# Kernel tuning notes

Measured on AMD Instinct MI355X. Metric: run time of the kernel, lower is better.

## Reference

```python
import jax, jax.numpy as jnp
import numpy as np

N = 50000      # nodes
E = 800000     # edges
NUM_STATIC = 8
T = 24         # dynamic seq len (in_features - num_static)
LH = 64        # lstm_hidden
C = 32         # n_hidden (per-head out channels)
H = 4          # heads
NC = 4         # num_classes
IN_GAT = LH + NUM_STATIC  # 72


def _uniform(key, shape, scale):
    return jax.random.uniform(key, shape, jnp.float32, -scale, scale)


def setup_inputs() -> dict:
    key = jax.random.key(0)
    ks = jax.random.split(key, 32)
    s1 = 1.0 / np.sqrt(LH)
    inp = {
        'x': jax.random.normal(ks[0], (N, NUM_STATIC + T), jnp.float32),
        'edge_index': jax.random.randint(ks[1], (2, E), 0, N, jnp.int64),
        'edge_attr': jax.random.uniform(ks[2], (E, 1), jnp.float32),
        # LSTM layer 0 (input_size=1), layer 1 (input_size=LH); gate order i,f,g,o
        'w_ih0': _uniform(ks[3], (4 * LH, 1), s1),
        'w_hh0': _uniform(ks[4], (4 * LH, LH), s1),
        'b_ih0': _uniform(ks[5], (4 * LH,), s1),
        'b_hh0': _uniform(ks[6], (4 * LH,), s1),
        'w_ih1': _uniform(ks[7], (4 * LH, LH), s1),
        'w_hh1': _uniform(ks[8], (4 * LH, LH), s1),
        'b_ih1': _uniform(ks[9], (4 * LH,), s1),
        'b_hh1': _uniform(ks[10], (4 * LH,), s1),
        # GATConv params (PyG: glorot lin, att vectors; bias zeros-init but randomize)
        'lin_w': _uniform(ks[11], (H * C, IN_GAT), np.sqrt(6.0 / (IN_GAT + H * C))),
        'lin_edge_w': _uniform(ks[12], (H * C, 1), np.sqrt(6.0 / (1 + H * C))),
        'att_src': _uniform(ks[13], (H, C), np.sqrt(6.0 / (C + 1))),
        'att_dst': _uniform(ks[14], (H, C), np.sqrt(6.0 / (C + 1))),
        'att_edge': _uniform(ks[15], (H, C), np.sqrt(6.0 / (C + 1))),
        'gat_bias': _uniform(ks[16], (H * C,), 0.1),
        # final Linear
        'fc_w': _uniform(ks[17], (NC, H * C), 1.0 / np.sqrt(H * C)),
        'fc_b': _uniform(ks[18], (NC,), 1.0 / np.sqrt(H * C)),
    }
    return inp


def _lstm_layer(x_seq, w_ih, w_hh, b_ih, b_hh):
    # x_seq: [N, T, D] -> hs: [N, T, LH]
    xw = jnp.einsum('ntd,gd->ntg', x_seq, w_ih) + b_ih + b_hh  # [N,T,4LH]
    n = x_seq.shape[0]
    h0 = jnp.zeros((n, w_hh.shape[1]), x_seq.dtype)

    def step(carry, xt):
        h, c = carry
        g = xt + h @ w_hh.T
        i, f, gg, o = jnp.split(g, 4, axis=-1)
        c = jax.nn.sigmoid(f) * c + jax.nn.sigmoid(i) * jnp.tanh(gg)
        h = jax.nn.sigmoid(o) * jnp.tanh(c)
        return (h, c), h

    _, hs = jax.lax.scan(step, (h0, h0), jnp.swapaxes(xw, 0, 1))
    return jnp.swapaxes(hs, 0, 1)


def reference(x, edge_index, edge_attr,
              w_ih0, w_hh0, b_ih0, b_hh0, w_ih1, w_hh1, b_ih1, b_hh1,
              lin_w, lin_edge_w, att_src, att_dst, att_edge, gat_bias,
              fc_w, fc_b):
    static = x[:, :NUM_STATIC]
    dyn = x[:, NUM_STATIC:, None]                      # [N,T,1]
    h1 = _lstm_layer(dyn, w_ih0, w_hh0, b_ih0, b_hh0)  # [N,T,LH] (eval: no dropout)
    h2 = _lstm_layer(h1, w_ih1, w_hh1, b_ih1, b_hh1)
    combined = jnp.concatenate([h2[:, -1, :], static], axis=1)  # [N, LH+NUM_STATIC]

    # --- GATConv (PyG defaults: add_self_loops=True, fill_value='mean') ---
    n = combined.shape[0]
    loop = jnp.arange(n, dtype=edge_index.dtype)
    src = jnp.concatenate([edge_index[0], loop])
    dst = jnp.concatenate([edge_index[1], loop])
    ea_mean = jnp.mean(edge_attr, axis=0, keepdims=True)        # [1,1]
    ea = jnp.concatenate([edge_attr, jnp.broadcast_to(ea_mean, (n, 1))], axis=0)

    xl = (combined @ lin_w.T).reshape(n, H, C)                  # [N,H,C]
    a_src = jnp.einsum('nhc,hc->nh', xl, att_src)               # [N,H]
    a_dst = jnp.einsum('nhc,hc->nh', xl, att_dst)
    e_emb = (ea @ lin_edge_w.T).reshape(-1, H, C)               # [Et,H,C]
    a_edge = jnp.einsum('ehc,hc->eh', e_emb, att_edge)          # [Et,H]

    logits = jax.nn.leaky_relu(a_src[src] + a_dst[dst] + a_edge, 0.2)  # [Et,H]
    m = jax.ops.segment_max(logits, dst, num_segments=n)
    ex = jnp.exp(logits - m[dst])
    denom = jax.ops.segment_sum(ex, dst, num_segments=n)
    alpha = ex / (denom[dst] + 1e-16)                           # [Et,H] (eval: no dropout)

    msg = xl[src] * alpha[:, :, None]                           # [Et,H,C]
    out = jax.ops.segment_sum(msg, dst, num_segments=n)         # [N,H,C]
    out = out.reshape(n, H * C) + gat_bias

    out = jax.nn.elu(out)
    return jax.nn.relu(out @ fc_w.T + fc_b)                     # [N,NC]
```

## Files before the change

kernel.cpp:

```cpp
#include <hip/hip_runtime.h>
#include <cstdint>

#define TT 24

typedef _Float16 half8 __attribute__((ext_vector_type(8)));
typedef float f32x4 __attribute__((ext_vector_type(4)));

static __device__ __forceinline__ float fsig(float x){
  float e = __builtin_amdgcn_exp2f(-1.44269504f*x);
  return __builtin_amdgcn_rcpf(1.0f + e);
}
static __device__ __forceinline__ float ftanh(float x){
  float e = __builtin_amdgcn_exp2f(-2.88539008f*x);
  return fmaf(2.0f, __builtin_amdgcn_rcpf(1.0f + e), -1.0f);
}
static __device__ __forceinline__ float lrelu(float x){ return x > 0.f ? x : 0.2f*x; }

static __device__ __forceinline__ int swzh(int b){ return b ^ (((b>>7)&7)<<4); }

__global__ void kPrep(const float* __restrict__ w_hh0, const float* __restrict__ w_ih1,
                      const float* __restrict__ w_hh1, const float* __restrict__ lin_w,
                      const float* __restrict__ lin_edge_w, const float* __restrict__ att_edge,
                      unsigned short* __restrict__ Bf,
                      float* __restrict__ linwT, float* __restrict__ cE)
{
  int gid = blockIdx.x*256 + threadIdx.x;
  if (gid < 49152){
    int mat = gid / 16384;
    int r = gid - mat*16384;
    int c = r>>13, nt = (r>>9)&15, l = (r>>3)&63, j = r&7;
    int k = c*32 + (l>>4)*8 + j;
    int col = nt*16 + (l&15);
    const float* wsrc = (mat==0) ? w_hh0 : (mat==1 ? w_ih1 : w_hh1);
    float v = wsrc[col*64 + k];
    union { _Float16 f; unsigned short u; } cv;
    cv.f = (_Float16)v;
    Bf[gid] = cv.u;
  }
  int g2 = gid - 49152;
  if (g2 >= 0 && g2 < 72*128){
    int k = g2 >> 7, ch = g2 & 127;
    linwT[g2] = lin_w[ch*72 + k];
  }
  if (gid >= 58368 && gid < 58372){
    int h = gid - 58368;
    float s = 0.f;
    for (int c=0;c<32;c++) s += lin_edge_w[h*32+c]*att_edge[h*32+c];
    cE[h] = s;
  }
}

__global__ __launch_bounds__(512) void kAB(const float* __restrict__ x,
    const unsigned short* __restrict__ Bf,
    const float* __restrict__ w_ih0, const float* __restrict__ b_ih0, const float* __restrict__ b_hh0,
    const float* __restrict__ b_ih1, const float* __restrict__ b_hh1,
    float* __restrict__ h2last, int N)
{
  __shared__ __align__(16) unsigned short sB[49152];
  __shared__ __align__(16) unsigned short sH1[4096];
  __shared__ __align__(16) unsigned short sH2[4096];
  __shared__ float sX[64*25];
  const int tid = threadIdx.x;
  const int wid = tid>>6, l = tid&63;
  const int wq = wid&3, wm = wid>>2;
  const int lr = l&15, lg = l>>4;
  const int nb = blockIdx.x*64;

  for (int i=tid; i<6144; i+=512)
    ((uint4*)sB)[i] = ((const uint4*)Bf)[i];
  for (int i=tid;i<1536;i+=512){
    int m = i/24, tt = i - m*24;
    int n = nb + m;
    sX[m*25+tt] = (n<N) ? x[(size_t)n*32 + 8 + tt] : 0.f;
  }
  for (int i=tid;i<4096;i+=512){ sH1[i]=0; sH2[i]=0; }

  float wih[4], bb0[4], bb1[4];
  #pragma unroll
  for (int nt=0;nt<4;nt++){
    int col = nt*64 + wq*16 + lr;
    wih[nt] = w_ih0[col];
    bb0[nt] = b_ih0[col] + b_hh0[col];
    bb1[nt] = b_ih1[col] + b_hh1[col];
  }
  float cc0[8], cc1[8];
  #pragma unroll
  for (int i=0;i<8;i++){ cc0[i]=0.f; cc1[i]=0.f; }
  __syncthreads();

  const char* h1B = (const char*)sH1;
  const char* h2B = (const char*)sH2;

  for (int t=0;t<TT;t++){
    f32x4 acc[2][4];
    #pragma unroll
    for (int mt=0;mt<2;mt++){
      #pragma unroll
      for (int r=0;r<4;r++){
        float xv = sX[(wm*32 + mt*16 + lg*4 + r)*25 + t];
        #pragma unroll
        for (int nt=0;nt<4;nt++) acc[mt][nt][r] = fmaf(xv, wih[nt], bb0[nt]);
      }
    }
    #pragma unroll
    for (int c=0;c<2;c++){
      half8 a[2];
      #pragma unroll
      for (int mt=0;mt<2;mt++){
        int by = swzh((wm*32 + mt*16 + lr)*128 + c*64 + lg*16);
        a[mt] = *(const half8*)(h1B + by);
      }
      #pragma unroll
      for (int nt=0;nt<4;nt++){
        half8 b = *(const half8*)&sB[((c*16 + nt*4 + wq)<<9) + l*8];
        #pragma unroll
        for (int mt=0;mt<2;mt++)
          acc[mt][nt] = __builtin_amdgcn_mfma_f32_16x16x32_f16(a[mt], b, acc[mt][nt], 0,0,0);
      }
    }
    __syncthreads();
    #pragma unroll
    for (int mt=0;mt<2;mt++){
      #pragma unroll
      for (int r=0;r<4;r++){
        int idx = mt*4+r, nd = wm*32 + mt*16 + lg*4 + r;
        float ig = fsig(acc[mt][0][r]), fg = fsig(acc[mt][1][r]);
        float gg = ftanh(acc[mt][2][r]), og = fsig(acc[mt][3][r]);
        cc0[idx] = fg*cc0[idx] + ig*gg;
        float h = og*ftanh(cc0[idx]);
        union { _Float16 f; unsigned short u; } cv; cv.f = (_Float16)h;
        *(unsigned short*)((char*)sH1 + swzh(nd*128 + (wq*16+lr)*2)) = cv.u;
      }
    }
    __syncthreads();
    #pragma unroll
    for (int mt=0;mt<2;mt++)
      #pragma unroll
      for (int nt=0;nt<4;nt++)
        #pragma unroll
        for (int r=0;r<4;r++) acc[mt][nt][r] = bb1[nt];
    #pragma unroll
    for (int c4=0;c4<4;c4++){
      const char* srcA = (c4<2) ? h1B : h2B;
      int cc = c4&1;
      int matB = (c4<2) ? 32 : 64;
      half8 a[2];
      #pragma unroll
      for (int mt=0;mt<2;mt++){
        int by = swzh((wm*32 + mt*16 + lr)*128 + cc*64 + lg*16);
        a[mt] = *(const half8*)(srcA + by);
      }
      #pragma unroll
      for (int nt=0;nt<4;nt++){
        half8 b = *(const half8*)&sB[((matB + cc*16 + nt*4 + wq)<<9) + l*8];
        #pragma unroll
        for (int mt=0;mt<2;mt++)
          acc[mt][nt] = __builtin_amdgcn_mfma_f32_16x16x32_f16(a[mt], b, acc[mt][nt], 0,0,0);
      }
    }
    __syncthreads();
    #pragma unroll
    for (int mt=0;mt<2;mt++){
      #pragma unroll
      for (int r=0;r<4;r++){
        int idx = mt*4+r, nd = wm*32 + mt*16 + lg*4 + r;
        float ig = fsig(acc[mt][0][r]), fg = fsig(acc[mt][1][r]);
        float gg = ftanh(acc[mt][2][r]), og = fsig(acc[mt][3][r]);
        cc1[idx] = fg*cc1[idx] + ig*gg;
        float h = og*ftanh(cc1[idx]);
        union { _Float16 f; unsigned short u; } cv; cv.f = (_Float16)h;
        *(unsigned short*)((char*)sH2 + swzh(nd*128 + (wq*16+lr)*2)) = cv.u;
        if (t == TT-1){
          int n = nb + nd;
          if (n < N) h2last[(size_t)n*64 + wq*16 + lr] = h;
        }
      }
    }
  }
}

__global__ __launch_bounds__(256) void kXL(const float* __restrict__ h2last, const float* __restrict__ x,
    const float* __restrict__ linwT, const float* __restrict__ att_src, const float* __restrict__ att_dst,
    float* __restrict__ xl, float* __restrict__ a_src, float* __restrict__ a_dst, int N)
{
  __shared__ float sLW[72*128];
  __shared__ float sC[16*72];
  const int tid = threadIdx.x;
  const int nb0 = blockIdx.x * 16;
  for (int i = tid*4; i < 9216; i += 1024)
    *(float4*)&sLW[i] = *(const float4*)&linwT[i];
  for (int i = tid; i < 16*64; i += 256){
    int m = i >> 6, k = i & 63; int n = nb0 + m;
    sC[m*72 + k] = (n < N) ? h2last[(size_t)n*64 + k] : 0.f;
  }
  if (tid < 128){
    int m = tid >> 3, j = tid & 7; int n = nb0 + m;
    sC[m*72 + 64 + j] = (n < N) ? x[(size_t)n*32 + j] : 0.f;
  }
  __syncthreads();
  const int ch = tid & 127, half = tid >> 7;
  float acc[8];
  #pragma unroll
  for (int m=0;m<8;m++) acc[m]=0.f;
  for (int k=0;k<72;k++){
    float w = sLW[k*128 + ch];
    #pragma unroll
    for (int m=0;m<8;m++) acc[m] += w * sC[(half*8+m)*72 + k];
  }
  float aS = att_src[ch], aD = att_dst[ch];
  int h = ch >> 5;
  #pragma unroll
  for (int m=0;m<8;m++){
    int n = nb0 + half*8 + m;
    float v = acc[m];
    float ps = v*aS, pd = v*aD;
    #pragma unroll
    for (int d=1; d<32; d<<=1){ ps += __shfl_xor(ps, d); pd += __shfl_xor(pd, d); }
    if (n < N){
      xl[(size_t)n*128 + ch] = v;
      if ((ch & 31) == 0){ a_src[n*4 + h] = ps; a_dst[n*4 + h] = pd; }
    }
  }
}

__global__ void kEa(const float* __restrict__ ea, float* __restrict__ acc, int E){
  int gid = blockIdx.x*blockDim.x + threadIdx.x;
  float s = 0.f;
  for (int i = gid; i < E; i += gridDim.x*blockDim.x) s += ea[i];
  #pragma unroll
  for (int d=1; d<64; d<<=1) s += __shfl_xor(s, d);
  if ((threadIdx.x & 63) == 0) atomicAdd(acc, s);
}

__global__ void kDeg(const int* __restrict__ dst, int* __restrict__ deg, int E, int N){
  int e = blockIdx.x*256 + threadIdx.x;
  if (e < E){
    unsigned d = (unsigned)dst[e];
    if (d < (unsigned)N) atomicAdd(&deg[d], 1);
  }
}

__global__ __launch_bounds__(1024) void kScan(const int* __restrict__ deg, int* __restrict__ ptrA,
                                              int* __restrict__ cursor, int N){
  __shared__ int sWS[16];
  __shared__ int sWO[16];
  const int tid = threadIdx.x;
  const int C = (N + 1 + 1023) / 1024;
  const int i0 = tid * C;
  int local = 0;
  for (int i = i0; i < i0 + C && i < N; i++) local += deg[i];
  int lane = tid & 63, wv = tid >> 6;
  int v = local;
  #pragma unroll
  for (int d=1; d<64; d<<=1){ int u = __shfl_up(v, d); if (lane >= d) v += u; }
  if (lane == 63) sWS[wv] = v;
  __syncthreads();
  if (tid < 16){
    int s = sWS[tid];
    int vv = s;
    #pragma unroll
    for (int d=1; d<16; d<<=1){ int u = __shfl_up(vv, d); if (tid >= d) vv += u; }
    sWO[tid] = vv - s;
  }
  __syncthreads();
  int run = sWO[wv] + (v - local);
  for (int i = i0; i < i0 + C; i++){
    if (i <= N){
      ptrA[i] = run;
      if (i < N){ cursor[i] = run; run += deg[i]; }
    }
  }
}

__global__ void kFill(const int* __restrict__ dst, int* __restrict__ cursor,
                      int* __restrict__ csr, int E, int N){
  int e = blockIdx.x*256 + threadIdx.x;
  if (e < E){
    unsigned d = (unsigned)dst[e];
    if (d < (unsigned)N){ int p = atomicAdd(&cursor[d], 1); csr[p] = e; }
  }
}

__global__ __launch_bounds__(256) void kAgg(const float* __restrict__ xl, const float* __restrict__ a_src,
    const float* __restrict__ a_dst, const int* __restrict__ esrc, const float* __restrict__ eattr,
    const int* __restrict__ ptrA, const int* __restrict__ csr, const float* __restrict__ cE,
    const float* __restrict__ eacc, const float* __restrict__ gat_bias, const float* __restrict__ fc_w,
    const float* __restrict__ fc_b, float* __restrict__ out, int N, int E)
{
  const int n = blockIdx.x*4 + (threadIdx.x >> 6);
  const int lane = threadIdx.x & 63;
  if (n >= N) return;
  float4 cEv = *(const float4*)cE;
  float eam = eacc[0] / (float)E;
  float4 ad  = *(const float4*)&a_dst[n*4];
  float4 asn = *(const float4*)&a_src[n*4];
  float sl0 = lrelu(asn.x + ad.x + eam*cEv.x);
  float sl1 = lrelu(asn.y + ad.y + eam*cEv.y);
  float sl2 = lrelu(asn.z + ad.z + eam*cEv.z);
  float sl3 = lrelu(asn.w + ad.w + eam*cEv.w);
  float mx0=sl0, mx1=sl1, mx2=sl2, mx3=sl3;
  const int p0 = ptrA[n], p1 = ptrA[n+1];
  for (int i = p0 + lane; i < p1; i += 64){
    int e = csr[i];
    int s = esrc[e];
    float ev = eattr[e];
    float4 av = *(const float4*)&a_src[s*4];
    mx0 = fmaxf(mx0, lrelu(av.x + ad.x + ev*cEv.x));
    mx1 = fmaxf(mx1, lrelu(av.y + ad.y + ev*cEv.y));
    mx2 = fmaxf(mx2, lrelu(av.z + ad.z + ev*cEv.z));
    mx3 = fmaxf(mx3, lrelu(av.w + ad.w + ev*cEv.w));
  }
  #pragma unroll
  for (int d=1; d<64; d<<=1){
    mx0 = fmaxf(mx0, __shfl_xor(mx0,d));
    mx1 = fmaxf(mx1, __shfl_xor(mx1,d));
    mx2 = fmaxf(mx2, __shfl_xor(mx2,d));
    mx3 = fmaxf(mx3, __shfl_xor(mx3,d));
  }
  const int ch0 = lane, ch1 = lane + 64;
  const int h0 = lane >> 5;
  float adh0 = h0 ? ad.y : ad.x,  adh1 = h0 ? ad.w : ad.z;
  float ceh0 = h0 ? cEv.y : cEv.x, ceh1 = h0 ? cEv.w : cEv.z;
  float mxh0 = h0 ? mx1 : mx0,    mxh1 = h0 ? mx3 : mx2;
  float slh0 = h0 ? sl1 : sl0,    slh1 = h0 ? sl3 : sl2;
  float pse0 = __expf(slh0 - mxh0), pse1 = __expf(slh1 - mxh1);
  float den0 = pse0, den1 = pse1;
  float acc0 = pse0 * xl[(size_t)n*128 + ch0];
  float acc1 = pse1 * xl[(size_t)n*128 + ch1];
  for (int i = p0; i < p1; i++){
    int e = csr[i];
    int s = esrc[e];
    float ev = eattr[e];
    float4 av = *(const float4*)&a_src[s*4];
    float avh0 = h0 ? av.y : av.x;
    float avh1 = h0 ? av.w : av.z;
    float pp0 = __expf(lrelu(avh0 + adh0 + ev*ceh0) - mxh0);
    float pp1 = __expf(lrelu(avh1 + adh1 + ev*ceh1) - mxh1);
    den0 += pp0; den1 += pp1;
    acc0 += pp0 * xl[(size_t)s*128 + ch0];
    acc1 += pp1 * xl[(size_t)s*128 + ch1];
  }
  float v0 = acc0/(den0 + 1e-16f) + gat_bias[ch0];
  float v1 = acc1/(den1 + 1e-16f) + gat_bias[ch1];
  v0 = v0 > 0.f ? v0 : __expf(v0) - 1.f;
  v1 = v1 > 0.f ? v1 : __expf(v1) - 1.f;
  #pragma unroll
  for (int o=0;o<4;o++){
    float p = fc_w[o*128 + ch0]*v0 + fc_w[o*128 + ch1]*v1;
    #pragma unroll
    for (int d=1; d<64; d<<=1) p += __shfl_xor(p, d);
    if (lane == 0) out[(size_t)n*4 + o] = fmaxf(p + fc_b[o], 0.f);
  }
}

extern "C" void kernel_launch(void* const* d_in, const int* in_sizes, int n_in,
                              void* d_out, int out_size, void* d_ws, size_t ws_size,
                              hipStream_t stream)
{
  (void)n_in; (void)out_size; (void)ws_size;
  const float* x          = (const float*)d_in[0];
  const int*   eidx       = (const int*)d_in[1];
  const float* eattr      = (const float*)d_in[2];
  const float* w_ih0      = (const float*)d_in[3];
  const float* w_hh0      = (const float*)d_in[4];
  const float* b_ih0      = (const float*)d_in[5];
  const float* b_hh0      = (const float*)d_in[6];
  const float* w_ih1      = (const float*)d_in[7];
  const float* w_hh1      = (const float*)d_in[8];
  const float* b_ih1      = (const float*)d_in[9];
  const float* b_hh1      = (const float*)d_in[10];
  const float* lin_w      = (const float*)d_in[11];
  const float* lin_edge_w = (const float*)d_in[12];
  const float* att_src    = (const float*)d_in[13];
  const float* att_dst    = (const float*)d_in[14];
  const float* att_edge   = (const float*)d_in[15];
  const float* gat_bias   = (const float*)d_in[16];
  const float* fc_w       = (const float*)d_in[17];
  const float* fc_b       = (const float*)d_in[18];
  float* out = (float*)d_out;

  const int N = in_sizes[0] / 32;
  const int E = in_sizes[1] / 2;
  const int* esrc = eidx;
  const int* edst = eidx + E;

  float* ws = (float*)d_ws;
  size_t o = 0;
  unsigned short* Bfrag = (unsigned short*)(ws + o); o += 24576;
  float* linwT  = ws + o; o += 72*128;
  float* cE     = ws + o; o += 4;
  float* eacc   = ws + o; o += 4;
  float* h2last = ws + o; o += (size_t)N*64;
  float* xl     = ws + o; o += (size_t)N*128;
  float* a_src  = ws + o; o += (size_t)N*4;
  float* a_dst  = ws + o; o += (size_t)N*4;
  int* deg      = (int*)(ws + o); o += (size_t)N;
  int* ptrA     = (int*)(ws + o); o += (size_t)N + 1;
  int* cursor   = (int*)(ws + o); o += (size_t)N;
  int* csr      = (int*)(ws + o); o += (size_t)E;

  hipMemsetAsync(deg, 0, (size_t)N*4, stream);
  hipMemsetAsync(eacc, 0, 4, stream);
  kPrep<<<229, 256, 0, stream>>>(w_hh0, w_ih1, w_hh1, lin_w, lin_edge_w, att_edge,
                                 Bfrag, linwT, cE);
  kEa<<<512, 256, 0, stream>>>(eattr, eacc, E);
  kDeg<<<(E+255)/256, 256, 0, stream>>>(edst, deg, E, N);
  kScan<<<1, 1024, 0, stream>>>(deg, ptrA, cursor, N);
  kFill<<<(E+255)/256, 256, 0, stream>>>(edst, cursor, csr, E, N);

  kAB<<<(N+63)/64, 512, 0, stream>>>(x, Bfrag, w_ih0, b_ih0, b_hh0,
                                     b_ih1, b_hh1, h2last, N);

  kXL<<<(N+15)/16, 256, 0, stream>>>(h2last, x, linwT, att_src, att_dst, xl, a_src, a_dst, N);
  kAgg<<<(N+3)/4, 256, 0, stream>>>(xl, a_src, a_dst, esrc, eattr, ptrA, csr, cE, eacc,
                                    gat_bias, fc_w, fc_b, out, N, E);
}
```

Baseline: 844.6 us.

## Keep LSTM weights in registers and store GAT features as fp16

The LSTM kernel now holds all three fp16 weight fragment sets in registers instead of copying 96KB into shared memory per block. Blocks shrink to 32 nodes and 256 threads, so LDS use drops and more blocks can be resident. Separately, the node feature matrix xl is written as packed fp16 with the two head-halves interleaved, which halves the gather bandwidth in the aggregation kernel. The costs are higher register pressure (24 half8 weight fragments per thread) and reduced precision in the aggregated features.

```diff
diff --git a/kernel.cpp b/kernel.cpp
--- a/kernel.cpp
+++ b/kernel.cpp
@@ -17,6 +17,12 @@
 static __device__ __forceinline__ float lrelu(float x){ return x > 0.f ? x : 0.2f*x; }
 
 static __device__ __forceinline__ int swzh(int b){ return b ^ (((b>>7)&7)<<4); }
+static __device__ __forceinline__ float h2f_lo(unsigned u){
+  union { unsigned short s; _Float16 f; } c; c.s = (unsigned short)(u & 0xFFFF); return (float)c.f;
+}
+static __device__ __forceinline__ float h2f_hi(unsigned u){
+  union { unsigned short s; _Float16 f; } c; c.s = (unsigned short)(u >> 16); return (float)c.f;
+}
 
 __global__ void kPrep(const float* __restrict__ w_hh0, const float* __restrict__ w_ih1,
                       const float* __restrict__ w_hh1, const float* __restrict__ lin_w,
@@ -50,30 +56,37 @@
   }
 }
 
-__global__ __launch_bounds__(512) void kAB(const float* __restrict__ x,
+__global__ __launch_bounds__(256) void kAB(const float* __restrict__ x,
     const unsigned short* __restrict__ Bf,
     const float* __restrict__ w_ih0, const float* __restrict__ b_ih0, const float* __restrict__ b_hh0,
     const float* __restrict__ b_ih1, const float* __restrict__ b_hh1,
     float* __restrict__ h2last, int N)
 {
-  __shared__ __align__(16) unsigned short sB[49152];
-  __shared__ __align__(16) unsigned short sH1[4096];
-  __shared__ __align__(16) unsigned short sH2[4096];
-  __shared__ float sX[64*25];
+  __shared__ __align__(16) unsigned short sH1[2048];
+  __shared__ __align__(16) unsigned short sH2[2048];
+  __shared__ float sX[32*25];
   const int tid = threadIdx.x;
-  const int wid = tid>>6, l = tid&63;
-  const int wq = wid&3, wm = wid>>2;
+  const int wq = tid>>6, l = tid&63;
   const int lr = l&15, lg = l>>4;
-  const int nb = blockIdx.x*64;
-
-  for (int i=tid; i<6144; i+=512)
-    ((uint4*)sB)[i] = ((const uint4*)Bf)[i];
-  for (int i=tid;i<1536;i+=512){
+  const int nb = blockIdx.x*32;
+
+  for (int i=tid;i<768;i+=256){
     int m = i/24, tt = i - m*24;
     int n = nb + m;
     sX[m*25+tt] = (n<N) ? x[(size_t)n*32 + 8 + tt] : 0.f;
   }
-  for (int i=tid;i<4096;i+=512){ sH1[i]=0; sH2[i]=0; }
+  for (int i=tid;i<2048;i+=256){ sH1[i]=0; sH2[i]=0; }
+
+  half8 w0[2][4], w1i[2][4], w1h[2][4];
+  #pragma unroll
+  for (int c=0;c<2;c++){
+    #pragma unroll
+    for (int nt=0;nt<4;nt++){
+      w0 [c][nt] = *(const half8*)&Bf[(( 0 + c*16 + nt*4 + wq)<<9) + l*8];
+      w1i[c][nt] = *(const half8*)&Bf[((32 + c*16 + nt*4 + wq)<<9) + l*8];
+      w1h[c][nt] = *(const half8*)&Bf[((64 + c*16 + nt*4 + wq)<<9) + l*8];
+    }
+  }
 
   float wih[4], bb0[4], bb1[4];
   #pragma unroll
@@ -97,7 +110,7 @@
     for (int mt=0;mt<2;mt++){
       #pragma unroll
       for (int r=0;r<4;r++){
-        float xv = sX[(wm*32 + mt*16 + lg*4 + r)*25 + t];
+        float xv = sX[(mt*16 + lg*4 + r)*25 + t];
         #pragma unroll
         for (int nt=0;nt<4;nt++) acc[mt][nt][r] = fmaf(xv, wih[nt], bb0[nt]);
       }
@@ -106,16 +119,13 @@
     for (int c=0;c<2;c++){
       half8 a[2];
       #pragma unroll
-      for (int mt=0;mt<2;mt++){
-        int by = swzh((wm*32 + mt*16 + lr)*128 + c*64 + lg*16);
-        a[mt] = *(const half8*)(h1B + by);
-      }
+      for (int mt=0;mt<2;mt++)
+        a[mt] = *(const half8*)(h1B + swzh((mt*16+lr)*128 + c*64 + lg*16));
       #pragma unroll
       for (int nt=0;nt<4;nt++){
-        half8 b = *(const half8*)&sB[((c*16 + nt*4 + wq)<<9) + l*8];
         #pragma unroll
         for (int mt=0;mt<2;mt++)
-          acc[mt][nt] = __builtin_amdgcn_mfma_f32_16x16x32_f16(a[mt], b, acc[mt][nt], 0,0,0);
+          acc[mt][nt] = __builtin_amdgcn_mfma_f32_16x16x32_f16(a[mt], w0[c][nt], acc[mt][nt], 0,0,0);
       }
     }
     __syncthreads();
@@ -123,7 +133,7 @@
     for (int mt=0;mt<2;mt++){
       #pragma unroll
       for (int r=0;r<4;r++){
-        int idx = mt*4+r, nd = wm*32 + mt*16 + lg*4 + r;
+        int idx = mt*4+r, nd = mt*16 + lg*4 + r;
         float ig = fsig(acc[mt][0][r]), fg = fsig(acc[mt][1][r]);
         float gg = ftanh(acc[mt][2][r]), og = fsig(acc[mt][3][r]);
         cc0[idx] = fg*cc0[idx] + ig*gg;
@@ -142,17 +152,14 @@
     #pragma unroll
     for (int c4=0;c4<4;c4++){
       const char* srcA = (c4<2) ? h1B : h2B;
-      int cc = c4&1;
-      int matB = (c4<2) ? 32 : 64;
+      const int cc = c4&1;
       half8 a[2];
       #pragma unroll
-      for (int mt=0;mt<2;mt++){
-        int by = swzh((wm*32 + mt*16 + lr)*128 + cc*64 + lg*16);
-        a[mt] = *(const half8*)(srcA + by);
-      }
+      for (int mt=0;mt<2;mt++)
+        a[mt] = *(const half8*)(srcA + swzh((mt*16+lr)*128 + cc*64 + lg*16));
       #pragma unroll
       for (int nt=0;nt<4;nt++){
-        half8 b = *(const half8*)&sB[((matB + cc*16 + nt*4 + wq)<<9) + l*8];
+        half8 b = (c4<2) ? w1i[cc][nt] : w1h[cc][nt];
         #pragma unroll
         for (int mt=0;mt<2;mt++)
           acc[mt][nt] = __builtin_amdgcn_mfma_f32_16x16x32_f16(a[mt], b, acc[mt][nt], 0,0,0);
@@ -163,7 +170,7 @@
     for (int mt=0;mt<2;mt++){
       #pragma unroll
       for (int r=0;r<4;r++){
-        int idx = mt*4+r, nd = wm*32 + mt*16 + lg*4 + r;
+        int idx = mt*4+r, nd = mt*16 + lg*4 + r;
         float ig = fsig(acc[mt][0][r]), fg = fsig(acc[mt][1][r]);
         float gg = ftanh(acc[mt][2][r]), og = fsig(acc[mt][3][r]);
         cc1[idx] = fg*cc1[idx] + ig*gg;
@@ -181,7 +188,7 @@
 
 __global__ __launch_bounds__(256) void kXL(const float* __restrict__ h2last, const float* __restrict__ x,
     const float* __restrict__ linwT, const float* __restrict__ att_src, const float* __restrict__ att_dst,
-    float* __restrict__ xl, float* __restrict__ a_src, float* __restrict__ a_dst, int N)
+    unsigned short* __restrict__ xlh, float* __restrict__ a_src, float* __restrict__ a_dst, int N)
 {
   __shared__ float sLW[72*128];
   __shared__ float sC[16*72];
@@ -217,7 +224,8 @@
     #pragma unroll
     for (int d=1; d<32; d<<=1){ ps += __shfl_xor(ps, d); pd += __shfl_xor(pd, d); }
     if (n < N){
-      xl[(size_t)n*128 + ch] = v;
+      union { _Float16 f; unsigned short u; } cv; cv.f = (_Float16)v;
+      xlh[(size_t)n*128 + (ch&63)*2 + (ch>>6)] = cv.u;
       if ((ch & 31) == 0){ a_src[n*4 + h] = ps; a_dst[n*4 + h] = pd; }
     }
   }
@@ -281,7 +289,8 @@
   }
 }
 
-__global__ __launch_bounds__(256) void kAgg(const float* __restrict__ xl, const float* __restrict__ a_src,
+__global__ __launch_bounds__(256) void kAgg(const unsigned short* __restrict__ xlh,
+    const float* __restrict__ a_src,
     const float* __restrict__ a_dst, const int* __restrict__ esrc, const float* __restrict__ eattr,
     const int* __restrict__ ptrA, const int* __restrict__ csr, const float* __restrict__ cE,
     const float* __restrict__ eacc, const float* __restrict__ gat_bias, const float* __restrict__ fc_w,
@@ -290,6 +299,7 @@
   const int n = blockIdx.x*4 + (threadIdx.x >> 6);
   const int lane = threadIdx.x & 63;
   if (n >= N) return;
+  const unsigned* xlp = (const unsigned*)xlh;
   float4 cEv = *(const float4*)cE;
   float eam = eacc[0] / (float)E;
   float4 ad  = *(const float4*)&a_dst[n*4];
@@ -325,8 +335,9 @@
   float slh0 = h0 ? sl1 : sl0,    slh1 = h0 ? sl3 : sl2;
   float pse0 = __expf(slh0 - mxh0), pse1 = __expf(slh1 - mxh1);
   float den0 = pse0, den1 = pse1;
-  float acc0 = pse0 * xl[(size_t)n*128 + ch0];
-  float acc1 = pse1 * xl[(size_t)n*128 + ch1];
+  unsigned un = xlp[(size_t)n*64 + lane];
+  float acc0 = pse0 * h2f_lo(un);
+  float acc1 = pse1 * h2f_hi(un);
   for (int i = p0; i < p1; i++){
     int e = csr[i];
     int s = esrc[e];
@@ -337,8 +348,9 @@
     float pp0 = __expf(lrelu(avh0 + adh0 + ev*ceh0) - mxh0);
     float pp1 = __expf(lrelu(avh1 + adh1 + ev*ceh1) - mxh1);
     den0 += pp0; den1 += pp1;
-    acc0 += pp0 * xl[(size_t)s*128 + ch0];
-    acc1 += pp1 * xl[(size_t)s*128 + ch1];
+    unsigned u = xlp[(size_t)s*64 + lane];
+    acc0 += pp0 * h2f_lo(u);
+    acc1 += pp1 * h2f_hi(u);
   }
   float v0 = acc0/(den0 + 1e-16f) + gat_bias[ch0];
   float v1 = acc1/(den1 + 1e-16f) + gat_bias[ch1];
@@ -391,7 +403,7 @@
   float* cE     = ws + o; o += 4;
   float* eacc   = ws + o; o += 4;
   float* h2last = ws + o; o += (size_t)N*64;
-  float* xl     = ws + o; o += (size_t)N*128;
+  unsigned short* xlh = (unsigned short*)(ws + o); o += (size_t)N*64;
   float* a_src  = ws + o; o += (size_t)N*4;
   float* a_dst  = ws + o; o += (size_t)N*4;
   int* deg      = (int*)(ws + o); o += (size_t)N;
@@ -408,10 +420,10 @@
   kScan<<<1, 1024, 0, stream>>>(deg, ptrA, cursor, N);
   kFill<<<(E+255)/256, 256, 0, stream>>>(edst, cursor, csr, E, N);
 
-  kAB<<<(N+63)/64, 512, 0, stream>>>(x, Bfrag, w_ih0, b_ih0, b_hh0,
+  kAB<<<(N+31)/32, 256, 0, stream>>>(x, Bfrag, w_ih0, b_ih0, b_hh0,
                                      b_ih1, b_hh1, h2last, N);
 
-  kXL<<<(N+15)/16, 256, 0, stream>>>(h2last, x, linwT, att_src, att_dst, xl, a_src, a_dst, N);
-  kAgg<<<(N+3)/4, 256, 0, stream>>>(xl, a_src, a_dst, esrc, eattr, ptrA, csr, cE, eacc,
+  kXL<<<(N+15)/16, 256, 0, stream>>>(h2last, x, linwT, att_src, att_dst, xlh, a_src, a_dst, N);
+  kAgg<<<(N+3)/4, 256, 0, stream>>>(xlh, a_src, a_dst, esrc, eattr, ptrA, csr, cE, eacc,
                                     gat_bias, fc_w, fc_b, out, N, E);
 }
```

Measured after the change: 865.8 us. 2.5% more time.
